# Optimization experiments

Hardware: AMD Instinct MI355X
Metric: run time of the kernel (lower is better)

Reference implementation:

```python
import jax, jax.numpy as jnp
import numpy as np

EPS = 1e-10


def setup_inputs() -> dict:
    key = jax.random.key(0)
    kx, ky = jax.random.split(key)
    x = jax.random.normal(kx, (8, 8192, 3), dtype=jnp.float32)
    y = jax.random.normal(ky, (8, 8192, 3), dtype=jnp.float32)
    return {"x": x, "y": y}


def reference(x, y):
    # x: (B, N, 3), y: (B, M, 3)
    xy = -2.0 * jnp.einsum("bnd,bmd->bnm", x, y)          # (B, N, M)
    xx = jnp.sum(x * x, axis=-1, keepdims=True)            # (B, N, 1)
    yy = jnp.sum(y * y, axis=-1, keepdims=True)            # (B, M, 1)
    dist = jnp.sqrt(xy + xx + jnp.swapaxes(yy, 1, 2) + EPS)  # (B, N, M)
    distance1 = jnp.min(dist, axis=2)                      # (B, N): x -> nearest y
    distance2 = jnp.min(dist, axis=1)                      # (B, M): y -> nearest x
    mean1 = jnp.mean(distance1, axis=-1)                   # (B,)
    mean2 = jnp.mean(distance2, axis=-1)                   # (B,)
    return jnp.sum(jnp.maximum(mean1, mean2))
```

## Files before the change

### kernel.cpp

```cpp
#include <hip/hip_runtime.h>


#define BB 8
#define NN 8192
#define NPTS (BB*NN)
#define BLK 256
#define CCOLS 1024
#define RROWS 512
#define CT (CCOLS/32)
#define RT 4

typedef __attribute__((ext_vector_type(8))) short bf16x8;
typedef __attribute__((ext_vector_type(16))) float f32x16;

__device__ __forceinline__ unsigned f2mono(float f) {
    unsigned u = __float_as_uint(f);
    return u ^ ((unsigned)((int)u >> 31) | 0x80000000u);
}
__device__ __forceinline__ float mono2f(unsigned m) {
    unsigned u = ((int)m >= 0) ? ~m : (m ^ 0x80000000u);
    return __uint_as_float(u);
}
__device__ __forceinline__ unsigned short bfh(float v) {
    unsigned u = __float_as_uint(v);
    u += 0x7FFFu + ((u >> 16) & 1u);
    return (unsigned short)(u >> 16);
}
__device__ __forceinline__ float bff(unsigned short h) {
    return __uint_as_float(((unsigned)h) << 16);
}

__device__ __forceinline__ void encA(float q0, float q1, float q2, unsigned short e[16]) {
    float v0 = -2.f*q0, v1 = -2.f*q1, v2 = -2.f*q2;
    float s2 = q0*q0 + q1*q1 + q2*q2;
    unsigned short h0 = bfh(v0), h1 = bfh(v1), h2 = bfh(v2);
    unsigned short l0 = bfh(v0 - bff(h0)), l1 = bfh(v1 - bff(h1)), l2 = bfh(v2 - bff(h2));
    unsigned short sh = bfh(s2), sl = bfh(s2 - bff(sh));
    const unsigned short one = 0x3F80;
    e[0]=h0; e[1]=h1; e[2]=h2; e[3]=l0; e[4]=l1; e[5]=l2; e[6]=h0; e[7]=h1;
    e[8]=h2; e[9]=sh; e[10]=sl; e[11]=one; e[12]=one; e[13]=0; e[14]=0; e[15]=0;
}
__device__ __forceinline__ void encB(float w0, float w1, float w2, unsigned short e[16]) {
    float s2 = w0*w0 + w1*w1 + w2*w2;
    unsigned short h0 = bfh(w0), h1 = bfh(w1), h2 = bfh(w2);
    unsigned short l0 = bfh(w0 - bff(h0)), l1 = bfh(w1 - bff(h1)), l2 = bfh(w2 - bff(h2));
    unsigned short sh = bfh(s2), sl = bfh(s2 - bff(sh));
    const unsigned short one = 0x3F80;
    e[0]=h0; e[1]=h1; e[2]=h2; e[3]=h0; e[4]=h1; e[5]=h2; e[6]=l0; e[7]=l1;
    e[8]=l2; e[9]=one; e[10]=one; e[11]=sh; e[12]=sl; e[13]=0; e[14]=0; e[15]=0;
}

__global__ __launch_bounds__(BLK, 4) void
main_kernel(const float* __restrict__ x, const float* __restrict__ y,
            unsigned* __restrict__ mind) {
    __shared__ unsigned short benc[CCOLS * 16];
    __shared__ unsigned colmin[CCOLS];
    const int dir = blockIdx.z;
    const int b   = blockIdx.y;
    const int rc  = blockIdx.x >> 3;
    const int cc  = blockIdx.x & 7;
    const float* A  = dir ? y : x;
    const float* Bp = dir ? x : y;
    const int tid = threadIdx.x;

#pragma unroll
    for (int s = 0; s < CCOLS / BLK; ++s) {
        int ci = tid + s * BLK;
        colmin[ci] = 0xFFFFFFFFu;
        int gi = b * NN + cc * CCOLS + ci;
        union { unsigned short e[16]; uint4 q[2]; } u;
        encB(Bp[3*gi], Bp[3*gi+1], Bp[3*gi+2], u.e);
        ((uint4*)benc)[ci*2]     = u.q[0];
        ((uint4*)benc)[ci*2 + 1] = u.q[1];
    }

    const int lane = tid & 63;
    const int w    = tid >> 6;
    const int m    = lane & 31;
    const int h    = lane >> 5;
    bf16x8 af[RT];
    const int rowbase = b * NN + rc * RROWS + w * (RT * 32);
#pragma unroll
    for (int t = 0; t < RT; ++t) {
        int r = rowbase + t * 32 + m;
        union { unsigned short e[16]; bf16x8 v[2]; } u;
        encA(A[3*r], A[3*r+1], A[3*r+2], u.e);
        af[t] = u.v[h];
    }
    __syncthreads();

    f32x16 zro;
#pragma unroll
    for (int i = 0; i < 16; ++i) zro[i] = 0.f;

    const bf16x8* bv = (const bf16x8*)benc;
    bf16x8 bf = bv[m*2 + h];
#pragma unroll 2
    for (int ct = 0; ct < CT; ++ct) {
        bf16x8 nxt = (ct + 1 < CT) ? bv[(ct+1)*64 + m*2 + h] : bf;
        f32x16 a0 = __builtin_amdgcn_mfma_f32_32x32x16_bf16(af[0], bf, zro, 0, 0, 0);
        f32x16 a1 = __builtin_amdgcn_mfma_f32_32x32x16_bf16(af[1], bf, zro, 0, 0, 0);
        f32x16 a2 = __builtin_amdgcn_mfma_f32_32x32x16_bf16(af[2], bf, zro, 0, 0, 0);
        f32x16 a3 = __builtin_amdgcn_mfma_f32_32x32x16_bf16(af[3], bf, zro, 0, 0, 0);
        float p = 3.4e38f;
#pragma unroll
        for (int r = 0; r < 16; ++r) {
            p = fminf(fminf(fminf(fminf(a0[r], a1[r]), a2[r]), a3[r]), p);
        }
        atomicMin(&colmin[ct*32 + m], f2mono(p));
        bf = nxt;
    }
    __syncthreads();

#pragma unroll
    for (int s = 0; s < CCOLS / BLK; ++s) {
        int ci = tid + s * BLK;
        atomicMin(&mind[dir * NPTS + b * NN + cc * CCOLS + ci], colmin[ci]);
    }
}

__global__ void fin_kernel(const unsigned* __restrict__ mind,
                           float* __restrict__ bsums, unsigned* __restrict__ counter,
                           float* __restrict__ out) {
    __shared__ float red[BLK / 64];
    const int grp = blockIdx.x >> 2;
    const int sl  = blockIdx.x & 3;
    const int t = threadIdx.x;
    const unsigned* md = mind + grp * NN;
    float s = 0.f;
#pragma unroll
    for (int k = 0; k < NN / 4 / BLK; ++k) {
        int i = sl * (NN / 4) + t + k * BLK;
        s += sqrtf(fmaxf(mono2f(md[i]), 0.f) + 1e-10f);
    }
    for (int off = 32; off; off >>= 1) s += __shfl_down(s, off, 64);
    if ((t & 63) == 0) red[t >> 6] = s;
    __syncthreads();
    if (t == 0) {
        float tot = 0.f;
        for (int ww = 0; ww < BLK / 64; ++ww) tot += red[ww];
        atomicAdd(&bsums[grp], tot);
        __threadfence();
        unsigned old = atomicAdd(counter, 1u);
        if (old == 63u) {
            float acc = 0.f;
            for (int bb = 0; bb < BB; ++bb) {
                float s0 = atomicAdd(&bsums[bb], 0.f);
                float s1 = atomicAdd(&bsums[BB + bb], 0.f);
                acc += fmaxf(s0, s1);
            }
            out[0] = acc * (1.0f / (float)NN);
        }
    }
}

extern "C" void kernel_launch(void* const* d_in, const int* in_sizes, int n_in,
                              void* d_out, int out_size, void* d_ws, size_t ws_size,
                              hipStream_t stream) {
    const float* x = (const float*)d_in[0];
    const float* y = (const float*)d_in[1];
    float* out = (float*)d_out;

    char* ws = (char*)d_ws;
    unsigned* mind = (unsigned*)ws;
    float* bsums = (float*)(mind + 2 * NPTS);
    unsigned* counter = (unsigned*)(bsums + 16);

    hipMemsetAsync(mind, 0xFF, 2 * NPTS * sizeof(unsigned), stream);
    hipMemsetAsync(bsums, 0, 17 * sizeof(float), stream);
    main_kernel<<<dim3(128, BB, 2), BLK, 0, stream>>>(x, y, mind);
    fin_kernel<<<64, BLK, 0, stream>>>(mind, bsums, counter, out);
}
```

Measured before the change: 105.3 us.

## Give each block full column ownership to drop global atomics and memsets

Each block now owns 256 columns and loops over all 8192 rows in 16 strips, keeping the encoded column fragments and running column minima in registers. This removes the LDS column encoding, the per-tile LDS atomics, the global atomicMin array, and both memsets. The block computes its sqrt-sum directly, and a single-block finalize reduces the 512 partials. The cost is only 512 blocks, each doing a long serial loop with A re-encoded from global memory in every strip, so parallelism drops and occupancy is bounded by a launch bound of 2.

```diff
diff --git a/kernel.cpp b/kernel.cpp
--- a/kernel.cpp
+++ b/kernel.cpp
@@ -3,12 +3,11 @@
 
 #define BB 8
 #define NN 8192
-#define NPTS (BB*NN)
 #define BLK 256
-#define CCOLS 1024
-#define RROWS 512
-#define CT (CCOLS/32)
+#define CCOLS 256
+#define CT 8
 #define RT 4
+#define STRIPS 16
 
 typedef __attribute__((ext_vector_type(8))) short bf16x8;
 typedef __attribute__((ext_vector_type(16))) float f32x16;
@@ -50,107 +49,93 @@
     e[8]=l2; e[9]=one; e[10]=one; e[11]=sh; e[12]=sl; e[13]=0; e[14]=0; e[15]=0;
 }
 
-__global__ __launch_bounds__(BLK, 4) void
+__global__ __launch_bounds__(BLK, 2) void
 main_kernel(const float* __restrict__ x, const float* __restrict__ y,
-            unsigned* __restrict__ mind) {
-    __shared__ unsigned short benc[CCOLS * 16];
+            float* __restrict__ bpart) {
     __shared__ unsigned colmin[CCOLS];
-    const int dir = blockIdx.z;
-    const int b   = blockIdx.y;
-    const int rc  = blockIdx.x >> 3;
-    const int cc  = blockIdx.x & 7;
+    __shared__ float red[4];
+    const int bi  = blockIdx.x;
+    const int dir = bi >> 8;
+    const int b   = (bi >> 5) & 7;
+    const int cc  = bi & 31;
     const float* A  = dir ? y : x;
     const float* Bp = dir ? x : y;
     const int tid = threadIdx.x;
+    const int lane = tid & 63, w = tid >> 6;
+    const int m = lane & 31, h = lane >> 5;
 
+    colmin[tid] = 0xFFFFFFFFu;
+
+    bf16x8 bf[CT];
 #pragma unroll
-    for (int s = 0; s < CCOLS / BLK; ++s) {
-        int ci = tid + s * BLK;
-        colmin[ci] = 0xFFFFFFFFu;
-        int gi = b * NN + cc * CCOLS + ci;
-        union { unsigned short e[16]; uint4 q[2]; } u;
-        encB(Bp[3*gi], Bp[3*gi+1], Bp[3*gi+2], u.e);
-        ((uint4*)benc)[ci*2]     = u.q[0];
-        ((uint4*)benc)[ci*2 + 1] = u.q[1];
+    for (int ct = 0; ct < CT; ++ct) {
+        int c = b * NN + cc * CCOLS + ct * 32 + m;
+        union { unsigned short e[16]; bf16x8 v[2]; } u;
+        encB(Bp[3*c], Bp[3*c+1], Bp[3*c+2], u.e);
+        bf[ct] = u.v[h];
     }
-
-    const int lane = tid & 63;
-    const int w    = tid >> 6;
-    const int m    = lane & 31;
-    const int h    = lane >> 5;
-    bf16x8 af[RT];
-    const int rowbase = b * NN + rc * RROWS + w * (RT * 32);
-#pragma unroll
-    for (int t = 0; t < RT; ++t) {
-        int r = rowbase + t * 32 + m;
-        union { unsigned short e[16]; bf16x8 v[2]; } u;
-        encA(A[3*r], A[3*r+1], A[3*r+2], u.e);
-        af[t] = u.v[h];
-    }
-    __syncthreads();
 
     f32x16 zro;
 #pragma unroll
     for (int i = 0; i < 16; ++i) zro[i] = 0.f;
 
-    const bf16x8* bv = (const bf16x8*)benc;
-    bf16x8 bf = bv[m*2 + h];
-#pragma unroll 2
+    float rm[CT];
+#pragma unroll
+    for (int ct = 0; ct < CT; ++ct) rm[ct] = 3.4e38f;
+
+#pragma unroll 1
+    for (int s = 0; s < STRIPS; ++s) {
+        bf16x8 af[RT];
+#pragma unroll
+        for (int t = 0; t < RT; ++t) {
+            int r = b * NN + s * 512 + w * 128 + t * 32 + m;
+            union { unsigned short e[16]; bf16x8 v[2]; } u;
+            encA(A[3*r], A[3*r+1], A[3*r+2], u.e);
+            af[t] = u.v[h];
+        }
+#pragma unroll
+        for (int ct = 0; ct < CT; ++ct) {
+            f32x16 a0 = __builtin_amdgcn_mfma_f32_32x32x16_bf16(af[0], bf[ct], zro, 0, 0, 0);
+            f32x16 a1 = __builtin_amdgcn_mfma_f32_32x32x16_bf16(af[1], bf[ct], zro, 0, 0, 0);
+            f32x16 a2 = __builtin_amdgcn_mfma_f32_32x32x16_bf16(af[2], bf[ct], zro, 0, 0, 0);
+            f32x16 a3 = __builtin_amdgcn_mfma_f32_32x32x16_bf16(af[3], bf[ct], zro, 0, 0, 0);
+            float p = rm[ct];
+#pragma unroll
+            for (int r = 0; r < 16; ++r) {
+                float t0 = fminf(fminf(a0[r], a1[r]), a2[r]);
+                p = fminf(fminf(t0, a3[r]), p);
+            }
+            rm[ct] = p;
+        }
+    }
+
+#pragma unroll
     for (int ct = 0; ct < CT; ++ct) {
-        bf16x8 nxt = (ct + 1 < CT) ? bv[(ct+1)*64 + m*2 + h] : bf;
-        f32x16 a0 = __builtin_amdgcn_mfma_f32_32x32x16_bf16(af[0], bf, zro, 0, 0, 0);
-        f32x16 a1 = __builtin_amdgcn_mfma_f32_32x32x16_bf16(af[1], bf, zro, 0, 0, 0);
-        f32x16 a2 = __builtin_amdgcn_mfma_f32_32x32x16_bf16(af[2], bf, zro, 0, 0, 0);
-        f32x16 a3 = __builtin_amdgcn_mfma_f32_32x32x16_bf16(af[3], bf, zro, 0, 0, 0);
-        float p = 3.4e38f;
-#pragma unroll
-        for (int r = 0; r < 16; ++r) {
-            p = fminf(fminf(fminf(fminf(a0[r], a1[r]), a2[r]), a3[r]), p);
-        }
-        atomicMin(&colmin[ct*32 + m], f2mono(p));
-        bf = nxt;
+        float p = fminf(rm[ct], __shfl_xor(rm[ct], 32, 64));
+        if (h == 0) atomicMin(&colmin[ct * 32 + m], f2mono(p));
     }
     __syncthreads();
 
+    float d = sqrtf(fmaxf(mono2f(colmin[tid]), 0.f) + 1e-10f);
 #pragma unroll
-    for (int s = 0; s < CCOLS / BLK; ++s) {
-        int ci = tid + s * BLK;
-        atomicMin(&mind[dir * NPTS + b * NN + cc * CCOLS + ci], colmin[ci]);
-    }
+    for (int off = 32; off; off >>= 1) d += __shfl_down(d, off, 64);
+    if (lane == 0) red[w] = d;
+    __syncthreads();
+    if (tid == 0) bpart[bi] = red[0] + red[1] + red[2] + red[3];
 }
 
-__global__ void fin_kernel(const unsigned* __restrict__ mind,
-                           float* __restrict__ bsums, unsigned* __restrict__ counter,
-                           float* __restrict__ out) {
-    __shared__ float red[BLK / 64];
-    const int grp = blockIdx.x >> 2;
-    const int sl  = blockIdx.x & 3;
+__global__ void fin_kernel(const float* __restrict__ bpart, float* __restrict__ out) {
+    __shared__ float g[16];
     const int t = threadIdx.x;
-    const unsigned* md = mind + grp * NN;
-    float s = 0.f;
+    float v = bpart[t];
 #pragma unroll
-    for (int k = 0; k < NN / 4 / BLK; ++k) {
-        int i = sl * (NN / 4) + t + k * BLK;
-        s += sqrtf(fmaxf(mono2f(md[i]), 0.f) + 1e-10f);
-    }
-    for (int off = 32; off; off >>= 1) s += __shfl_down(s, off, 64);
-    if ((t & 63) == 0) red[t >> 6] = s;
+    for (int off = 16; off; off >>= 1) v += __shfl_down(v, off, 32);
+    if ((t & 31) == 0) g[t >> 5] = v;
     __syncthreads();
     if (t == 0) {
-        float tot = 0.f;
-        for (int ww = 0; ww < BLK / 64; ++ww) tot += red[ww];
-        atomicAdd(&bsums[grp], tot);
-        __threadfence();
-        unsigned old = atomicAdd(counter, 1u);
-        if (old == 63u) {
-            float acc = 0.f;
-            for (int bb = 0; bb < BB; ++bb) {
-                float s0 = atomicAdd(&bsums[bb], 0.f);
-                float s1 = atomicAdd(&bsums[BB + bb], 0.f);
-                acc += fmaxf(s0, s1);
-            }
-            out[0] = acc * (1.0f / (float)NN);
-        }
+        float acc = 0.f;
+        for (int b = 0; b < BB; ++b) acc += fmaxf(g[b], g[BB + b]);
+        out[0] = acc * (1.0f / (float)NN);
     }
 }
 
@@ -160,14 +145,8 @@
     const float* x = (const float*)d_in[0];
     const float* y = (const float*)d_in[1];
     float* out = (float*)d_out;
+    float* bpart = (float*)d_ws;
 
-    char* ws = (char*)d_ws;
-    unsigned* mind = (unsigned*)ws;
-    float* bsums = (float*)(mind + 2 * NPTS);
-    unsigned* counter = (unsigned*)(bsums + 16);
-
-    hipMemsetAsync(mind, 0xFF, 2 * NPTS * sizeof(unsigned), stream);
-    hipMemsetAsync(bsums, 0, 17 * sizeof(float), stream);
-    main_kernel<<<dim3(128, BB, 2), BLK, 0, stream>>>(x, y, mind);
-    fin_kernel<<<64, BLK, 0, stream>>>(mind, bsums, counter, out);
+    main_kernel<<<512, BLK, 0, stream>>>(x, y, bpart);
+    fin_kernel<<<1, 512, 0, stream>>>(bpart, out);
 }
```

Result: slower. 119.5 us (+13.5%).
